# Kernel tuning notes

Measured on AMD Instinct MI355X. Metric: run time of the kernel, lower is better.

Reference implementation:

```python
import jax, jax.numpy as jnp
import numpy as np

EPS = 1e-12

def setup_inputs() -> dict:
    key = jax.random.key(0)
    k1, k2, k3, k4, k5, k6 = jax.random.split(key, 6)
    B, DIM, T = 16, 256, 2048
    K, D = 1024, 64  # num_embeddings, embedding_dim
    N = B * T
    input_data = jax.random.normal(k1, (B, DIM, T), dtype=jnp.float32)
    codebooks = jax.random.normal(k2, (K, D), dtype=jnp.float32)
    W_in = jax.random.normal(k3, (DIM, D), dtype=jnp.float32) / np.sqrt(DIM)
    b_in = jnp.zeros((D,), dtype=jnp.float32)
    W_out = jax.random.normal(k4, (D, DIM), dtype=jnp.float32) / np.sqrt(D)
    b_out = jnp.zeros((DIM,), dtype=jnp.float32)
    random_vector = jax.random.normal(k5, (N, D), dtype=jnp.float32)
    return {"input_data": input_data, "codebooks": codebooks,
            "W_in": W_in, "b_in": b_in, "W_out": W_out, "b_out": b_out,
            "random_vector": random_vector}

def reference(input_data, codebooks, W_in, b_in, W_out, b_out, random_vector):
    B, DIM, T = input_data.shape
    D = codebooks.shape[1]
    # encode: [B, DIM, T] -> [B, T, DIM] -> project -> [B*T, D]
    x = jnp.einsum('bct,cd->btd', input_data, W_in) + b_in
    x = x.reshape(-1, D)  # [N, D]
    distances = (jnp.sum(x * x, axis=1, keepdims=True)
                 - 2.0 * (x @ codebooks.T)
                 + jnp.sum(codebooks * codebooks, axis=1)[None, :])  # [N, K]
    min_indices = jnp.argmin(distances, axis=1)  # [N]
    hard = codebooks[min_indices]  # [N, D]
    # noise substitution
    norm_resid = jnp.sqrt(jnp.sum((x - hard) ** 2, axis=1, keepdims=True))
    norm_rand = jnp.sqrt(jnp.sum(random_vector ** 2, axis=1, keepdims=True))
    vq_error = (norm_resid / (norm_rand + EPS)) * random_vector
    q = x + vq_error  # [N, D]
    # decode: [N, D] -> [B, T, D] -> project_out -> [B, DIM, T]
    q = q.reshape(B, T, D)
    out = jnp.einsum('btd,dc->bct', q, W_out) + b_out[None, :, None]
    return out
```

## Files before the change

### kernel.cpp

```cpp
#include <hip/hip_runtime.h>
#include <hip/hip_bf16.h>

typedef __bf16 bf16x8 __attribute__((ext_vector_type(8)));
typedef unsigned short u16x8 __attribute__((ext_vector_type(8)));
typedef unsigned short u16x4 __attribute__((ext_vector_type(4)));
typedef float f32x4 __attribute__((ext_vector_type(4)));
typedef unsigned short u16;

constexpr int DIMc = 256, Tt = 2048, Kk = 1024, Dd = 64;

#define WS_WINT 0
#define WS_CBX  16896
#define WS_WOX  90624
#define WS_CN_F 54528

__device__ __forceinline__ u16 f2b(float f) {
  unsigned u = __float_as_uint(f);
  return (u16)((u + 0x7FFFu + ((u >> 16) & 1u)) >> 16);
}
__device__ __forceinline__ f32x4 mfma16(u16x8 a, u16x8 b, f32x4 c) {
  return __builtin_amdgcn_mfma_f32_16x16x32_bf16(
      __builtin_bit_cast(bf16x8, a), __builtin_bit_cast(bf16x8, b), c, 0, 0, 0);
}
__device__ __forceinline__ void dma16(const u16* g, u16* l) {
  __builtin_amdgcn_global_load_lds(
      (const __attribute__((address_space(1))) unsigned int*)g,
      (__attribute__((address_space(3))) unsigned int*)l, 16, 0, 0);
}

__global__ void nsvq_prep(const float* __restrict__ cb, const float* __restrict__ Win,
                          const float* __restrict__ Wout, u16* __restrict__ wsu) {
  const int g = blockIdx.x * 256 + threadIdx.x;
  for (int i = g; i < 16384; i += 8192) {
    int c = i >> 6, d = i & 63;
    wsu[WS_WINT + d * 264 + c] = f2b(Win[i]);
  }
  for (int i = g; i < 65536; i += 8192) {
    int k = i >> 6, d = i & 63;
    wsu[WS_CBX + k * 72 + d] = f2b(-2.f * cb[i]);
  }
  for (int i = g; i < 16384; i += 8192) {
    int d = i >> 8, c = i & 255;
    wsu[WS_WOX + c * 72 + d] = f2b(Wout[i]);
  }
  if (g < 1024) {
    const float4* cr = (const float4*)(cb + (size_t)g * 64);
    float cn = 0.f;
    #pragma unroll
    for (int q = 0; q < 16; ++q) {
      float4 v = cr[q];
      cn = fmaf(v.x, v.x, fmaf(v.y, v.y, fmaf(v.z, v.z, fmaf(v.w, v.w, cn))));
    }
    ((float*)wsu)[WS_CN_F + g] = cn;
  }
}

__global__ __launch_bounds__(256, 2) void nsvq_main(
    const float* __restrict__ in, const float* __restrict__ rnd,
    const float* __restrict__ bin, const float* __restrict__ bout,
    const u16* __restrict__ wsu, const float* __restrict__ cnorm,
    float* __restrict__ out) {
  __shared__ u16 buf[18432];
  __shared__ u16 InT[64 * 256];
  __shared__ u16 Xt[64 * 64];
  __shared__ float mnp[4][64];

  const int tid  = threadIdx.x;
  const int lane = tid & 63;
  const int w    = tid >> 6;
  const int quad = lane >> 4, col = lane & 15;
  const int b  = blockIdx.x >> 5;
  const int t0 = (blockIdx.x & 31) << 6;
  const int myt = w * 16 + col;

  {
    const float* ib = in + (size_t)b * DIMc * Tt + t0 + lane;
    #pragma unroll
    for (int it = 0; it < 8; ++it) {
      int c0 = w * 64 + it * 8;
      u16x8 pk;
      #pragma unroll
      for (int j = 0; j < 8; ++j) pk[j] = f2b(ib[(size_t)(c0 + j) * Tt]);
      *(u16x8*)(InT + lane * 256 + (((c0 >> 3) ^ (lane & 7)) << 3)) = pk;
    }
  }
  #pragma unroll
  for (int ii = 0; ii < 9; ++ii) {
    int i = w + 4 * ii;
    if (i < 33) dma16(wsu + WS_WINT + i * 512 + lane * 8, buf + i * 512);
  }
  __syncthreads();

  f32x4 acc[4];
  {
    u16x8 Bf[8];
    #pragma unroll
    for (int kt = 0; kt < 8; ++kt)
      Bf[kt] = *(const u16x8*)(InT + myt * 256 + (((kt * 4 + quad) ^ (myt & 7)) << 3));
    #pragma unroll
    for (int mt = 0; mt < 4; ++mt) {
      acc[mt] = *(const f32x4*)(bin + mt * 16 + quad * 4);
      #pragma unroll
      for (int kt = 0; kt < 8; ++kt) {
        u16x8 A = *(const u16x8*)(buf + (mt * 16 + col) * 264 + kt * 32 + quad * 8);
        acc[mt] = mfma16(A, Bf[kt], acc[mt]);
      }
    }
  }
  float x2v = 0.f;
  #pragma unroll
  for (int mt = 0; mt < 4; ++mt) {
    u16x4 pk;
    #pragma unroll
    for (int r = 0; r < 4; ++r) { x2v = fmaf(acc[mt][r], acc[mt][r], x2v); pk[r] = f2b(acc[mt][r]); }
    int bk = mt * 2 + (quad >> 1);
    *(u16x4*)(Xt + myt * 64 + ((bk ^ (myt & 7)) << 3) + (quad & 1) * 4) = pk;
  }
  x2v += __shfl_xor(x2v, 16);
  x2v += __shfl_xor(x2v, 32);
  __syncthreads();

  const float* rp = rnd + ((size_t)(b * Tt) + t0 + myt) * Dd;
  f32x4 rv[4];
  #pragma unroll
  for (int mt = 0; mt < 4; ++mt) rv[mt] = *(const f32x4*)(rp + mt * 16 + quad * 4);

  u16x8 Xa[4], Xb[4];
  #pragma unroll
  for (int nt = 0; nt < 4; ++nt) {
    int tr = nt * 16 + col;
    Xa[nt] = *(const u16x8*)(Xt + tr * 64 + ((quad ^ (tr & 7)) << 3));
    Xb[nt] = *(const u16x8*)(Xt + tr * 64 + (((4 + quad) ^ (tr & 7)) << 3));
  }
  float minv[4] = {3.4e38f, 3.4e38f, 3.4e38f, 3.4e38f};
  {
    #pragma unroll
    for (int ii = 0; ii < 5; ++ii) {
      int i = w + 4 * ii;
      if (i < 18) dma16(wsu + WS_CBX + i * 512 + lane * 8, buf + i * 512);
    }
    for (int ch = 0; ch < 8; ++ch) {
      __syncthreads();
      if (ch < 7) {
        const u16* src = wsu + WS_CBX + (ch + 1) * 9216;
        u16* dst = buf + ((ch + 1) & 1) * 9216;
        #pragma unroll
        for (int ii = 0; ii < 5; ++ii) {
          int i = w + 4 * ii;
          if (i < 18) dma16(src + i * 512 + lane * 8, dst + i * 512);
        }
      }
      const u16* cbase = buf + (ch & 1) * 9216;
      #pragma unroll
      for (int ms = 0; ms < 2; ++ms) {
        f32x4 cn = *(const f32x4*)(cnorm + ch * 128 + w * 32 + ms * 16 + quad * 4);
        const u16* ar = cbase + (w * 32 + ms * 16 + col) * 72;
        u16x8 A0 = *(const u16x8*)(ar + quad * 8);
        u16x8 A1 = *(const u16x8*)(ar + 32 + quad * 8);
        #pragma unroll
        for (int nt = 0; nt < 4; ++nt) {
          f32x4 a = cn;
          a = mfma16(A0, Xa[nt], a);
          a = mfma16(A1, Xb[nt], a);
          #pragma unroll
          for (int r = 0; r < 4; ++r) minv[nt] = fminf(minv[nt], a[r]);
        }
      }
    }
  }
  #pragma unroll
  for (int nt = 0; nt < 4; ++nt) {
    float m = minv[nt];
    m = fminf(m, __shfl_xor(m, 16));
    m = fminf(m, __shfl_xor(m, 32));
    mnp[w][nt * 16 + col] = m;
  }
  __syncthreads();

  #pragma unroll
  for (int ii = 0; ii < 9; ++ii) {
    int i = w + 4 * ii;
    dma16(wsu + WS_WOX + i * 512 + lane * 8, buf + i * 512);
  }
  float rr2v = 0.f;
  #pragma unroll
  for (int mt = 0; mt < 4; ++mt)
    #pragma unroll
    for (int r = 0; r < 4; ++r) rr2v = fmaf(rv[mt][r], rv[mt][r], rr2v);
  rr2v += __shfl_xor(rr2v, 16);
  rr2v += __shfl_xor(rr2v, 32);
  float mv = fminf(fminf(mnp[0][myt], mnp[1][myt]), fminf(mnp[2][myt], mnp[3][myt]));
  float r2  = fmaxf(x2v + mv, 0.f);
  float scv = sqrtf(r2) / (sqrtf(rr2v) + 1e-12f);
  #pragma unroll
  for (int mt = 0; mt < 4; ++mt) {
    u16x4 pk;
    #pragma unroll
    for (int r = 0; r < 4; ++r) pk[r] = f2b(fmaf(scv, rv[mt][r], acc[mt][r]));
    int bk = mt * 2 + (quad >> 1);
    *(u16x4*)(Xt + myt * 64 + ((bk ^ (myt & 7)) << 3) + (quad & 1) * 4) = pk;
  }
  __syncthreads();

  u16x8 Q0 = *(const u16x8*)(Xt + myt * 64 + ((quad ^ (myt & 7)) << 3));
  u16x8 Q1 = *(const u16x8*)(Xt + myt * 64 + (((4 + quad) ^ (myt & 7)) << 3));
  float* ob0 = out + (size_t)b * DIMc * Tt + t0 + myt;
  #pragma unroll
  for (int mt = 0; mt < 16; ++mt) {
    f32x4 a = *(const f32x4*)(bout + mt * 16 + quad * 4);
    const u16* ar = buf + (mt * 16 + col) * 72;
    u16x8 A0 = *(const u16x8*)(ar + quad * 8);
    u16x8 A1 = *(const u16x8*)(ar + 32 + quad * 8);
    a = mfma16(A0, Q0, a);
    a = mfma16(A1, Q1, a);
    #pragma unroll
    for (int r = 0; r < 4; ++r) ob0[(size_t)(mt * 16 + quad * 4 + r) * Tt] = a[r];
  }
}

extern "C" void kernel_launch(void* const* d_in, const int* in_sizes, int n_in,
                              void* d_out, int out_size, void* d_ws, size_t ws_size,
                              hipStream_t stream) {
  const float *in = nullptr, *cb = nullptr, *rnd = nullptr, *bin = nullptr, *bout = nullptr;
  const float* w16[2] = {nullptr, nullptr}; int nw = 0;
  for (int i = 0; i < n_in; ++i) {
    switch (in_sizes[i]) {
      case 8388608: in  = (const float*)d_in[i]; break;
      case 65536:   cb  = (const float*)d_in[i]; break;
      case 2097152: rnd = (const float*)d_in[i]; break;
      case 64:      bin = (const float*)d_in[i]; break;
      case 256:     bout= (const float*)d_in[i]; break;
      case 16384:   if (nw < 2) w16[nw++] = (const float*)d_in[i]; break;
      default: break;
    }
  }
  if (!in)  in  = (const float*)d_in[0];
  if (!cb)  cb  = (const float*)d_in[1];
  if (nw < 2) { w16[0] = (const float*)d_in[2]; w16[1] = (const float*)d_in[4]; }
  if (!bin) bin = (const float*)d_in[3];
  if (!bout) bout = (const float*)d_in[5];
  if (!rnd) rnd = (const float*)d_in[6];

  u16* wsu = (u16*)d_ws;
  const float* cnorm = (const float*)d_ws + WS_CN_F;
  float* outp = (float*)d_out;

  nsvq_prep<<<32, 256, 0, stream>>>(cb, w16[0], w16[1], wsu);
  nsvq_main<<<512, 256, 0, stream>>>(in, rnd, bin, bout, wsu, cnorm, outp);
}
```

Before: 126.5 us.

## Read weights and codebook straight from global memory instead of LDS staging

The main kernel no longer stages W_in, the codebook and W_out into a 36KB shared buffer through global_load_lds DMA. Each lane now loads its MFMA A-fragments directly from the workspace, which is expected to be served from cache, and the codebook loop prefetches the next fragment into registers. This removes the per-chunk barriers and lowers LDS use per block, which may allow more resident blocks. The prep kernel's transposing writes are also reordered so the stores are coalesced. The risk is more global and L2 traffic, since every wave reads the full codebook, and global-load latency that the register prefetch may not fully hide.

```diff
diff --git a/kernel.cpp b/kernel.cpp
--- a/kernel.cpp
+++ b/kernel.cpp
@@ -22,26 +22,21 @@
   return __builtin_amdgcn_mfma_f32_16x16x32_bf16(
       __builtin_bit_cast(bf16x8, a), __builtin_bit_cast(bf16x8, b), c, 0, 0, 0);
 }
-__device__ __forceinline__ void dma16(const u16* g, u16* l) {
-  __builtin_amdgcn_global_load_lds(
-      (const __attribute__((address_space(1))) unsigned int*)g,
-      (__attribute__((address_space(3))) unsigned int*)l, 16, 0, 0);
-}
 
 __global__ void nsvq_prep(const float* __restrict__ cb, const float* __restrict__ Win,
                           const float* __restrict__ Wout, u16* __restrict__ wsu) {
   const int g = blockIdx.x * 256 + threadIdx.x;
   for (int i = g; i < 16384; i += 8192) {
-    int c = i >> 6, d = i & 63;
-    wsu[WS_WINT + d * 264 + c] = f2b(Win[i]);
+    int d = i >> 8, c = i & 255;
+    wsu[WS_WINT + d * 264 + c] = f2b(Win[c * 64 + d]);
   }
   for (int i = g; i < 65536; i += 8192) {
     int k = i >> 6, d = i & 63;
     wsu[WS_CBX + k * 72 + d] = f2b(-2.f * cb[i]);
   }
   for (int i = g; i < 16384; i += 8192) {
-    int d = i >> 8, c = i & 255;
-    wsu[WS_WOX + c * 72 + d] = f2b(Wout[i]);
+    int c = i >> 6, d = i & 63;
+    wsu[WS_WOX + c * 72 + d] = f2b(Wout[d * 256 + c]);
   }
   if (g < 1024) {
     const float4* cr = (const float4*)(cb + (size_t)g * 64);
@@ -60,7 +55,6 @@
     const float* __restrict__ bin, const float* __restrict__ bout,
     const u16* __restrict__ wsu, const float* __restrict__ cnorm,
     float* __restrict__ out) {
-  __shared__ u16 buf[18432];
   __shared__ u16 InT[64 * 256];
   __shared__ u16 Xt[64 * 64];
   __shared__ float mnp[4][64];
@@ -84,11 +78,6 @@
       *(u16x8*)(InT + lane * 256 + (((c0 >> 3) ^ (lane & 7)) << 3)) = pk;
     }
   }
-  #pragma unroll
-  for (int ii = 0; ii < 9; ++ii) {
-    int i = w + 4 * ii;
-    if (i < 33) dma16(wsu + WS_WINT + i * 512 + lane * 8, buf + i * 512);
-  }
   __syncthreads();
 
   f32x4 acc[4];
@@ -100,9 +89,10 @@
     #pragma unroll
     for (int mt = 0; mt < 4; ++mt) {
       acc[mt] = *(const f32x4*)(bin + mt * 16 + quad * 4);
+      const u16* ar = wsu + WS_WINT + (mt * 16 + col) * 264 + quad * 8;
       #pragma unroll
       for (int kt = 0; kt < 8; ++kt) {
-        u16x8 A = *(const u16x8*)(buf + (mt * 16 + col) * 264 + kt * 32 + quad * 8);
+        u16x8 A = *(const u16x8*)(ar + kt * 32);
         acc[mt] = mfma16(A, Bf[kt], acc[mt]);
       }
     }
@@ -134,38 +124,30 @@
   }
   float minv[4] = {3.4e38f, 3.4e38f, 3.4e38f, 3.4e38f};
   {
-    #pragma unroll
-    for (int ii = 0; ii < 5; ++ii) {
-      int i = w + 4 * ii;
-      if (i < 18) dma16(wsu + WS_CBX + i * 512 + lane * 8, buf + i * 512);
-    }
-    for (int ch = 0; ch < 8; ++ch) {
-      __syncthreads();
-      if (ch < 7) {
-        const u16* src = wsu + WS_CBX + (ch + 1) * 9216;
-        u16* dst = buf + ((ch + 1) & 1) * 9216;
+    const u16* cb0 = wsu + WS_CBX + (w * 32 + col) * 72 + quad * 8;
+    const float* cn0 = cnorm + w * 32 + quad * 4;
+    u16x8 A0 = *(const u16x8*)(cb0);
+    u16x8 A1 = *(const u16x8*)(cb0 + 32);
+    f32x4 cn = *(const f32x4*)(cn0);
+    #pragma unroll
+    for (int it = 0; it < 16; ++it) {
+      u16x8 nA0, nA1; f32x4 ncn;
+      if (it < 15) {
+        int nx = it + 1;
+        int off = ((nx >> 1) << 7) + ((nx & 1) << 4);
+        nA0 = *(const u16x8*)(cb0 + off * 72);
+        nA1 = *(const u16x8*)(cb0 + off * 72 + 32);
+        ncn = *(const f32x4*)(cn0 + off);
+      }
+      #pragma unroll
+      for (int nt = 0; nt < 4; ++nt) {
+        f32x4 a = cn;
+        a = mfma16(A0, Xa[nt], a);
+        a = mfma16(A1, Xb[nt], a);
         #pragma unroll
-        for (int ii = 0; ii < 5; ++ii) {
-          int i = w + 4 * ii;
-          if (i < 18) dma16(src + i * 512 + lane * 8, dst + i * 512);
-        }
+        for (int r = 0; r < 4; ++r) minv[nt] = fminf(minv[nt], a[r]);
       }
-      const u16* cbase = buf + (ch & 1) * 9216;
-      #pragma unroll
-      for (int ms = 0; ms < 2; ++ms) {
-        f32x4 cn = *(const f32x4*)(cnorm + ch * 128 + w * 32 + ms * 16 + quad * 4);
-        const u16* ar = cbase + (w * 32 + ms * 16 + col) * 72;
-        u16x8 A0 = *(const u16x8*)(ar + quad * 8);
-        u16x8 A1 = *(const u16x8*)(ar + 32 + quad * 8);
-        #pragma unroll
-        for (int nt = 0; nt < 4; ++nt) {
-          f32x4 a = cn;
-          a = mfma16(A0, Xa[nt], a);
-          a = mfma16(A1, Xb[nt], a);
-          #pragma unroll
-          for (int r = 0; r < 4; ++r) minv[nt] = fminf(minv[nt], a[r]);
-        }
-      }
+      A0 = nA0; A1 = nA1; cn = ncn;
     }
   }
   #pragma unroll
@@ -177,11 +159,6 @@
   }
   __syncthreads();
 
-  #pragma unroll
-  for (int ii = 0; ii < 9; ++ii) {
-    int i = w + 4 * ii;
-    dma16(wsu + WS_WOX + i * 512 + lane * 8, buf + i * 512);
-  }
   float rr2v = 0.f;
   #pragma unroll
   for (int mt = 0; mt < 4; ++mt)
@@ -200,7 +177,6 @@
     int bk = mt * 2 + (quad >> 1);
     *(u16x4*)(Xt + myt * 64 + ((bk ^ (myt & 7)) << 3) + (quad & 1) * 4) = pk;
   }
-  __syncthreads();
 
   u16x8 Q0 = *(const u16x8*)(Xt + myt * 64 + ((quad ^ (myt & 7)) << 3));
   u16x8 Q1 = *(const u16x8*)(Xt + myt * 64 + (((4 + quad) ^ (myt & 7)) << 3));
@@ -208,9 +184,9 @@
   #pragma unroll
   for (int mt = 0; mt < 16; ++mt) {
     f32x4 a = *(const f32x4*)(bout + mt * 16 + quad * 4);
-    const u16* ar = buf + (mt * 16 + col) * 72;
-    u16x8 A0 = *(const u16x8*)(ar + quad * 8);
-    u16x8 A1 = *(const u16x8*)(ar + 32 + quad * 8);
+    const u16* ar = wsu + WS_WOX + (mt * 16 + col) * 72 + quad * 8;
+    u16x8 A0 = *(const u16x8*)(ar);
+    u16x8 A1 = *(const u16x8*)(ar + 32);
     a = mfma16(A0, Q0, a);
     a = mfma16(A1, Q1, a);
     #pragma unroll
```

After: 128.4 us. About the same (+1.5%).
